# Kernel optimization log

Hardware: AMD Instinct MI355X
Metric: run time of the kernel (lower is better)

## Reference

```python
import jax, jax.numpy as jnp
import numpy as np
import math

FMAPS = [(80, 0.06), (40, 0.12), (20, 0.24), (10, 0.48), (5, 0.72)]
SPLITS = [0, 6400, 8000, 8400, 8500, 8525]
N_LEVELS = 5
N_CAND = 9
ALPHA_REG = 1.0   # config.reg_weights
GAMMA, F_ALPHA = 2.0, 0.25


def _make_priors():
    ps = []
    for f, s in FMAPS:
        c = (np.arange(f, dtype=np.float32) + 0.5) / f
        cy, cx = np.meshgrid(c, c, indexing="ij")
        ps.append(np.stack([cx.ravel(), cy.ravel(),
                            np.full(f * f, s, np.float32),
                            np.full(f * f, s, np.float32)], 1))
    return jnp.asarray(np.concatenate(ps, 0))


def cxcy_to_xy(b):
    return jnp.concatenate([b[..., :2] - b[..., 2:] / 2, b[..., :2] + b[..., 2:] / 2], -1)


def xy_to_cxcy(b):
    return jnp.concatenate([(b[..., :2] + b[..., 2:]) / 2, b[..., 2:] - b[..., :2]], -1)


def gcxgcy_to_cxcy(g, priors):
    cxcy = g[..., :2] * priors[..., 2:] / 10.0 + priors[..., :2]
    wh = jnp.exp(g[..., 2:] / 5.0) * priors[..., 2:]
    return jnp.concatenate([cxcy, wh], -1)


def iou_matrix(a, b):  # a [K,4] corners, b [P,4] corners -> [K,P]
    lt = jnp.maximum(a[:, None, :2], b[None, :, :2])
    rb = jnp.minimum(a[:, None, 2:], b[None, :, 2:])
    wh = jnp.clip(rb - lt, 0.0)
    inter = wh[..., 0] * wh[..., 1]
    area_a = (a[:, 2] - a[:, 0]) * (a[:, 3] - a[:, 1])
    area_b = (b[:, 2] - b[:, 0]) * (b[:, 3] - b[:, 1])
    return inter / (area_a[:, None] + area_b[None, :] - inter)


def _assign_image(boxes_i, labels_i, locs_i, priors):
    # boxes_i [K,4] xyxy, labels_i [K] int, locs_i [P,4] encoded offsets
    gt_cxcy = xy_to_cxcy(boxes_i)
    per_level, pos_ov_all = [], []
    for l in range(N_LEVELS):
        pl = priors[SPLITS[l]:SPLITS[l + 1]]                       # [Pl,4] cxcywh
        dist = jnp.linalg.norm(gt_cxcy[:, None, :2] - pl[None, :, :2], axis=-1)  # [K,Pl]
        _, top_idx = jax.lax.top_k(-dist, N_CAND)                  # [K,9] closest priors
        ov = iou_matrix(boxes_i, cxcy_to_xy(pl))                   # [K,Pl]
        pos_ov = jnp.take_along_axis(ov, top_idx, axis=1)          # [K,9]
        pos_ov_all.append(pos_ov)
        per_level.append((pl, top_idx, pos_ov, locs_i[SPLITS[l]:SPLITS[l + 1]]))
    cat = jnp.concatenate(pos_ov_all, 1)                           # [K, 5*9]
    thr = cat.mean(1) + jnp.std(cat, axis=1, ddof=1)               # torch.std is unbiased

    labels_out, gt_match, dec_match, valid_all = [], [], [], []
    for l, (pl, top_idx, pos_ov, locs_l) in enumerate(per_level):
        cand = pl[top_idx]                                          # [K,9,4]
        inside = ((boxes_i[:, None, 0] < cand[..., 0]) & (cand[..., 0] < boxes_i[:, None, 2]) &
                  (boxes_i[:, None, 1] < cand[..., 1]) & (cand[..., 1] < boxes_i[:, None, 3]))
        cand_pos = (pos_ov > thr[:, None]) & inside                 # [K,9]
        masked = jnp.where(cand_pos, pos_ov, 0.0)                   # loop init current_max_iou=0
        best_ob = jnp.argmax(masked, axis=0)                        # [9], first-max == strict-> loop
        best_iou = jnp.max(masked, axis=0)
        valid = best_iou > 0.0                                      # [9]
        lab = jnp.where(valid, labels_i[best_ob], 0)
        Pl = SPLITS[l + 1] - SPLITS[l]
        # NB: original code indexes label array by candidate index c (bug kept faithfully)
        labels_out.append(jnp.zeros(Pl, jnp.int32).at[jnp.arange(N_CAND)].set(lab))
        decoded = cxcy_to_xy(gcxgcy_to_cxcy(locs_l, pl))            # [Pl,4]
        prior_idx = top_idx[best_ob, jnp.arange(N_CAND)]            # [9]
        dec_match.append(decoded[prior_idx])
        gt_match.append(boxes_i[best_ob])
        valid_all.append(valid)
    return (jnp.concatenate(labels_out),                            # [P]
            jnp.concatenate(gt_match, 0),                           # [45,4]
            jnp.concatenate(dec_match, 0),                          # [45,4]
            jnp.concatenate(valid_all))                             # [45]


def _ciou(pred, gt):  # corner boxes [N,4]
    w1, h1 = pred[:, 2] - pred[:, 0], pred[:, 3] - pred[:, 1]
    w2, h2 = gt[:, 2] - gt[:, 0], gt[:, 3] - gt[:, 1]
    lt = jnp.maximum(pred[:, :2], gt[:, :2]); rb = jnp.minimum(pred[:, 2:], gt[:, 2:])
    wh = jnp.clip(rb - lt, 0.0)
    inter = wh[:, 0] * wh[:, 1]
    union = w1 * h1 + w2 * h2 - inter
    iou = inter / union
    c1 = (pred[:, :2] + pred[:, 2:]) / 2; c2 = (gt[:, :2] + gt[:, 2:]) / 2
    rho2 = jnp.sum((c1 - c2) ** 2, -1)
    clt = jnp.minimum(pred[:, :2], gt[:, :2]); crb = jnp.maximum(pred[:, 2:], gt[:, 2:])
    cdiag = jnp.sum((crb - clt) ** 2, -1)
    v = (4.0 / math.pi ** 2) * (jnp.arctan(w2 / h2) - jnp.arctan(w1 / h1)) ** 2
    alpha = jax.lax.stop_gradient(v / (1.0 - iou + v))
    return jnp.clip(iou - rho2 / cdiag - alpha * v, -1.0, 1.0)


def _focal(logits, targets):  # logits [N,C], targets [N] in {0..C}, 0=background
    C = logits.shape[-1]
    cls = jnp.arange(1, C + 1)
    t = targets[:, None]
    p = jax.nn.sigmoid(logits)
    term1 = (1.0 - p) ** GAMMA * jax.nn.log_sigmoid(logits)
    term2 = p ** GAMMA * jax.nn.log_sigmoid(-logits)
    pos = (t == cls).astype(logits.dtype)
    neg = ((t != cls) & (t >= 0)).astype(logits.dtype)
    return -jnp.sum(pos * F_ALPHA * term1 + neg * (1.0 - F_ALPHA) * term2)


def setup_inputs():
    key = jax.random.key(0)
    k1, k2, k3, k4, k5 = jax.random.split(key, 5)
    B, K, C, P = 32, 16, 80, 8525
    lo = jax.random.uniform(k1, (B, K, 2), minval=0.05, maxval=0.55)
    sz = jax.random.uniform(k2, (B, K, 2), minval=0.08, maxval=0.35)
    boxes = jnp.concatenate([lo, lo + sz], -1)
    labels = jax.random.randint(k3, (B, K), 1, C + 1, dtype=jnp.int32)
    predicted_locs = jax.random.normal(k4, (B, P, 4), jnp.float32)
    predicted_scores = jax.random.normal(k5, (B, P, C), jnp.float32)
    return {"predicted_locs": predicted_locs, "predicted_scores": predicted_scores,
            "boxes": boxes, "labels": labels, "priors_cxcy": _make_priors()}


def reference(predicted_locs, predicted_scores, boxes, labels, priors_cxcy):
    tc, gt_m, dec_m, valid = jax.vmap(_assign_image, in_axes=(0, 0, 0, None))(
        boxes, labels, predicted_locs, priors_cxcy)
    tc_flat = tc.reshape(-1)
    n_pos = jnp.sum(tc_flat > 0).astype(jnp.float32)
    conf_loss = _focal(predicted_scores.reshape(-1, predicted_scores.shape[-1]), tc_flat) / n_pos
    ci = _ciou(dec_m.reshape(-1, 4), gt_m.reshape(-1, 4))
    vm = valid.reshape(-1).astype(jnp.float32)
    loc_loss = jnp.sum((1.0 - ci) * vm) / jnp.maximum(vm.sum(), 1.0)
    return conf_loss + ALPHA_REG * loc_loss
```

## Files before the change

### kernel.cpp

```cpp
#include <hip/hip_runtime.h>
#include <math.h>

#define KGT   16
#define NCAND 9
#define NLVL  5
#define NPRI  8525
#define NCLS  80
#define NIMG  32

#define FOCAL_BLOCKS 2016
#define TOTAL_BLOCKS (FOCAL_BLOCKS + NIMG)
#define NELEM (NIMG * NPRI * NCLS)
#define N4    (NELEM / 4)
#define CHUNK 2707
#define NROUND 11

#define OFF_IMG 8192

typedef float f4v __attribute__((ext_vector_type(4)));

__device__ __forceinline__ float focal_elem(float x)
{
    float e  = __expf(-fabsf(x));
    float t  = 1.f + e;
    float r  = __builtin_amdgcn_rcpf(t);
    float sp = fmaxf(x, 0.f) + __logf(t);
    float nm = (x >= 0.f) ? 1.f : e;
    float p  = nm * r;
    return p * p * sp;
}

__device__ __forceinline__ float focal4v(f4v v)
{
    return focal_elem(v.x) + focal_elem(v.y) + focal_elem(v.z) + focal_elem(v.w);
}

__global__ __launch_bounds__(256)
void atss_main(const float* __restrict__ locs,
               const float* __restrict__ scores,
               const float* __restrict__ boxes,
               const int*   __restrict__ labels,
               const float* __restrict__ priors,
               float* __restrict__ partials,
               float* __restrict__ imgstats)
{
    const int tid = threadIdx.x;
    const int blk = blockIdx.x;

    __shared__ float wsum[4];
    __shared__ float pov[KGT * 45];
    __shared__ int   tix[KGT * 45];
    __shared__ float sbox[KGT][4];
    __shared__ int   slab[KGT];
    __shared__ float thr[KGT];
    __shared__ float rc, rl;
    __shared__ int   rn;

    if (blk < FOCAL_BLOCKS) {
        const f4v* s4 = (const f4v*)scores;
        const int cbase = blk * CHUNK;

        f4v buf[3];
        #pragma unroll
        for (int k = 0; k < 3; ++k)
            buf[k] = __builtin_nontemporal_load(
                         s4 + min(cbase + k * 256 + tid, N4 - 1));

        float a0 = 0.f, a1 = 0.f;
        #pragma unroll
        for (int k = 0; k < NROUND; ++k) {
            f4v v = buf[k % 3];
            if (k + 3 < NROUND)
                buf[k % 3] = __builtin_nontemporal_load(
                                 s4 + min(cbase + (k + 3) * 256 + tid, N4 - 1));
            bool vld = (k * 256 + tid < CHUNK) && (cbase + k * 256 + tid < N4);
            float tv = focal4v(v);
            if (k & 1) a1 += vld ? tv : 0.f;
            else       a0 += vld ? tv : 0.f;
        }

        float lsum = a0 + a1;
        #pragma unroll
        for (int off = 32; off > 0; off >>= 1) lsum += __shfl_down(lsum, off);
        if ((tid & 63) == 0) wsum[tid >> 6] = lsum;
        __syncthreads();
        if (tid == 0)
            partials[blk] = wsum[0] + wsum[1] + wsum[2] + wsum[3];
        return;
    }

    const int b = blk - FOCAL_BLOCKS;
    const int SPLc[6] = {0, 6400, 8000, 8400, 8500, 8525};
    const int FDIM[5] = {80, 40, 20, 10, 5};

    if (tid == 0) { rc = 0.f; rl = 0.f; rn = 0; }
    if (tid < KGT) {
        float4 bxv = ((const float4*)boxes)[b * KGT + tid];
        sbox[tid][0] = bxv.x; sbox[tid][1] = bxv.y;
        sbox[tid][2] = bxv.z; sbox[tid][3] = bxv.w;
        slab[tid] = labels[b * KGT + tid];
    }
    __syncthreads();

    if (tid < KGT * NLVL) {
        const int g = tid / NLVL;
        const int l = tid % NLVL;
        const int f    = FDIM[l];
        const int base = SPLc[l];
        const float gcx = (sbox[g][0] + sbox[g][2]) * 0.5f;
        const float gcy = (sbox[g][1] + sbox[g][3]) * 0.5f;

        const float ff = (float)f;
        int ix0 = (int)floorf(gcx * ff); ix0 = min(max(ix0, 0), f - 1);
        int iy0 = (int)floorf(gcy * ff); iy0 = min(max(iy0, 0), f - 1);
        int sx = min(max(ix0 - 2, 0), f - 5);
        int sy = min(max(iy0 - 2, 0), f - 5);

        unsigned long long L[NCAND];
        #pragma unroll
        for (int s = 0; s < NCAND; ++s) L[s] = ~0ull;

        for (int dy = 0; dy < 5; ++dy) {
            for (int dx = 0; dx < 5; ++dx) {
                int idx = (sy + dy) * f + (sx + dx);
                float2 pc = ((const float2*)priors)[(base + idx) * 2];
                float ddx = gcx - pc.x, ddy = gcy - pc.y;
                float dist = sqrtf(ddx * ddx + ddy * ddy);
                unsigned long long pk =
                    ((unsigned long long)__float_as_uint(dist) << 32) | (unsigned)idx;
                if (pk < L[NCAND - 1]) {
                    L[NCAND - 1] = pk;
                    #pragma unroll
                    for (int s = NCAND - 1; s >= 1; --s) {
                        if (L[s] < L[s - 1]) {
                            unsigned long long tw = L[s]; L[s] = L[s - 1]; L[s - 1] = tw;
                        } else break;
                    }
                }
            }
        }
        #pragma unroll
        for (int s = 0; s < NCAND; ++s) {
            int idx = (int)(unsigned)(L[s] & 0xffffffffull);
            float4 pr = ((const float4*)priors)[base + idx];
            float px0 = pr.x - pr.z * 0.5f, py0 = pr.y - pr.w * 0.5f;
            float px1 = pr.x + pr.z * 0.5f, py1 = pr.y + pr.w * 0.5f;
            float iw = fmaxf(fminf(sbox[g][2], px1) - fmaxf(sbox[g][0], px0), 0.f);
            float ih = fmaxf(fminf(sbox[g][3], py1) - fmaxf(sbox[g][1], py0), 0.f);
            float inter = iw * ih;
            float areaA = (sbox[g][2] - sbox[g][0]) * (sbox[g][3] - sbox[g][1]);
            float areaP = (px1 - px0) * (py1 - py0);
            int o = g * 45 + l * NCAND + s;
            pov[o] = inter / (areaA + areaP - inter);
            tix[o] = idx;
        }
    }
    __syncthreads();

    if (tid < KGT) {
        float s = 0.f;
        for (int q = 0; q < 45; ++q) s += pov[tid * 45 + q];
        float mean = s / 45.f;
        float ss = 0.f;
        for (int q = 0; q < 45; ++q) { float d = pov[tid * 45 + q] - mean; ss += d * d; }
        thr[tid] = mean + sqrtf(ss / 44.f);
    }
    __syncthreads();

    if (tid < NLVL * NCAND) {
        int l = tid / NCAND, j = tid % NCAND;
        float bestv = -1.f; int bestg = 0;
        #pragma unroll
        for (int gg = 0; gg < KGT; ++gg) {
            float m = pov[gg * 45 + tid];
            int pi = tix[gg * 45 + tid];
            float4 pr = ((const float4*)priors)[SPLc[l] + pi];
            bool inside = (sbox[gg][0] < pr.x) && (pr.x < sbox[gg][2]) &&
                          (sbox[gg][1] < pr.y) && (pr.y < sbox[gg][3]);
            float mm = ((m > thr[gg]) && inside) ? m : 0.f;
            if (mm > bestv) { bestv = mm; bestg = gg; }
        }
        if (bestv > 0.f) {
            int lab = slab[bestg];
            long pos = (long)b * NPRI + SPLc[l] + j;
            float x  = scores[pos * NCLS + (lab - 1)];
            float e  = expf(-fabsf(x));
            float l1 = log1pf(e);
            float spp = fmaxf(x, 0.f) + l1;
            float spn = fmaxf(-x, 0.f) + l1;
            float p   = (x >= 0.f) ? 1.f / (1.f + e) : e / (1.f + e);
            float corr = 0.25f * (1.f - p) * (1.f - p) * spn - 0.75f * p * p * spp;

            int pi = tix[bestg * 45 + tid];
            float4 pr = ((const float4*)priors)[SPLc[l] + pi];
            float4 lc = ((const float4*)locs)[b * NPRI + SPLc[l] + pi];
            float cx = lc.x * pr.z / 10.f + pr.x;
            float cy = lc.y * pr.w / 10.f + pr.y;
            float w  = expf(lc.z / 5.f) * pr.z;
            float h  = expf(lc.w / 5.f) * pr.w;
            float qx0 = cx - w * 0.5f, qy0 = cy - h * 0.5f;
            float qx1 = cx + w * 0.5f, qy1 = cy + h * 0.5f;
            float gx0 = sbox[bestg][0], gy0 = sbox[bestg][1];
            float gx1 = sbox[bestg][2], gy1 = sbox[bestg][3];
            float w1 = qx1 - qx0, h1 = qy1 - qy0, w2 = gx1 - gx0, h2 = gy1 - gy0;
            float iw = fmaxf(fminf(qx1, gx1) - fmaxf(qx0, gx0), 0.f);
            float ih = fmaxf(fminf(qy1, gy1) - fmaxf(qy0, gy0), 0.f);
            float inter = iw * ih;
            float iou = inter / (w1 * h1 + w2 * h2 - inter);
            float dcx = (qx0 + qx1) * 0.5f - (gx0 + gx1) * 0.5f;
            float dcy = (qy0 + qy1) * 0.5f - (gy0 + gy1) * 0.5f;
            float rho2 = dcx * dcx + dcy * dcy;
            float ex = fmaxf(qx1, gx1) - fminf(qx0, gx0);
            float ey = fmaxf(qy1, gy1) - fminf(qy0, gy0);
            float cdiag = ex * ex + ey * ey;
            float da = atanf(w2 / h2) - atanf(w1 / h1);
            float v  = 0.4052847345693511f * da * da;
            float alpha = v / (1.f - iou + v);
            float ci = iou - rho2 / cdiag - alpha * v;
            ci = fminf(fmaxf(ci, -1.f), 1.f);

            atomicAdd(&rc, corr);
            atomicAdd(&rl, 1.f - ci);
            atomicAdd(&rn, 1);
        }
    }
    __syncthreads();
    if (tid == 0) {
        imgstats[b * 3 + 0] = rc;
        imgstats[b * 3 + 1] = rl;
        imgstats[b * 3 + 2] = (float)rn;
    }
}

__global__ __launch_bounds__(256)
void atss_finalize(const float* __restrict__ partials,
                   const float* __restrict__ imgstats,
                   float* __restrict__ out)
{
    const int tid = threadIdx.x;
    __shared__ float wsum[4];
    float lsum = 0.f;
    for (int i = tid; i < FOCAL_BLOCKS; i += 256) lsum += partials[i];
    #pragma unroll
    for (int off = 32; off > 0; off >>= 1) lsum += __shfl_down(lsum, off);
    if ((tid & 63) == 0) wsum[tid >> 6] = lsum;
    __syncthreads();
    if (tid == 0) {
        float base = 0.75f * (wsum[0] + wsum[1] + wsum[2] + wsum[3]);
        float corr = 0.f, loc = 0.f, cnt = 0.f;
        for (int b = 0; b < NIMG; ++b) {
            corr += imgstats[b * 3 + 0];
            loc  += imgstats[b * 3 + 1];
            cnt  += imgstats[b * 3 + 2];
        }
        float conf = (base + corr) / cnt;
        float locl = loc / fmaxf(cnt, 1.f);
        out[0] = conf + locl;
    }
}

extern "C" void kernel_launch(void* const* d_in, const int* in_sizes, int n_in,
                              void* d_out, int out_size, void* d_ws, size_t ws_size,
                              hipStream_t stream)
{
    const float* locs   = (const float*)d_in[0];
    const float* scores = (const float*)d_in[1];
    const float* boxes  = (const float*)d_in[2];
    const int*   labels = (const int*)d_in[3];
    const float* priors = (const float*)d_in[4];
    float* out = (float*)d_out;

    float* partials = (float*)d_ws;
    float* imgstats = (float*)((char*)d_ws + OFF_IMG);

    atss_main<<<TOTAL_BLOCKS, 256, 0, stream>>>(locs, scores, boxes, labels,
                                                priors, partials, imgstats);
    atss_finalize<<<1, 256, 0, stream>>>(partials, imgstats, out);
}
```

Measured before the change: 155.2 us.

## Replace chunked prefetch focal loop with simple grid-stride float4 loop

The focal-loss blocks now walk the scores with a grid-stride loop of plain float4 loads, replacing the per-block contiguous chunks that used a three-deep manual prefetch buffer, nontemporal loads and clamped indices. Each step now has the whole grid reading adjacent addresses. This drops the index clamping, validity masking and register buffering, but loses the explicit software prefetch and the nontemporal cache hint, leaving latency hiding to occupancy. Work split and results are otherwise unchanged.

```diff
diff --git a/kernel.cpp b/kernel.cpp
--- a/kernel.cpp
+++ b/kernel.cpp
@@ -12,12 +12,9 @@
 #define TOTAL_BLOCKS (FOCAL_BLOCKS + NIMG)
 #define NELEM (NIMG * NPRI * NCLS)
 #define N4    (NELEM / 4)
-#define CHUNK 2707
-#define NROUND 11
+#define FSTRIDE (FOCAL_BLOCKS * 256)
 
 #define OFF_IMG 8192
-
-typedef float f4v __attribute__((ext_vector_type(4)));
 
 __device__ __forceinline__ float focal_elem(float x)
 {
@@ -30,7 +27,7 @@
     return p * p * sp;
 }
 
-__device__ __forceinline__ float focal4v(f4v v)
+__device__ __forceinline__ float focal4(float4 v)
 {
     return focal_elem(v.x) + focal_elem(v.y) + focal_elem(v.z) + focal_elem(v.w);
 }
@@ -57,29 +54,11 @@
     __shared__ int   rn;
 
     if (blk < FOCAL_BLOCKS) {
-        const f4v* s4 = (const f4v*)scores;
-        const int cbase = blk * CHUNK;
-
-        f4v buf[3];
-        #pragma unroll
-        for (int k = 0; k < 3; ++k)
-            buf[k] = __builtin_nontemporal_load(
-                         s4 + min(cbase + k * 256 + tid, N4 - 1));
-
-        float a0 = 0.f, a1 = 0.f;
-        #pragma unroll
-        for (int k = 0; k < NROUND; ++k) {
-            f4v v = buf[k % 3];
-            if (k + 3 < NROUND)
-                buf[k % 3] = __builtin_nontemporal_load(
-                                 s4 + min(cbase + (k + 3) * 256 + tid, N4 - 1));
-            bool vld = (k * 256 + tid < CHUNK) && (cbase + k * 256 + tid < N4);
-            float tv = focal4v(v);
-            if (k & 1) a1 += vld ? tv : 0.f;
-            else       a0 += vld ? tv : 0.f;
-        }
-
-        float lsum = a0 + a1;
+        const float4* s4 = (const float4*)scores;
+        float lsum = 0.f;
+        for (int i = blk * 256 + tid; i < N4; i += FSTRIDE)
+            lsum += focal4(s4[i]);
+
         #pragma unroll
         for (int off = 32; off > 0; off >>= 1) lsum += __shfl_down(lsum, off);
         if ((tid & 63) == 0) wsum[tid >> 6] = lsum;
```

Measured after the change: 155.7 us. About the same (+0.3%).
